# Optimization experiments

Measured on AMD Instinct MI355X. Metric: run time of the kernel, lower is better.

Reference implementation:

```python
import jax, jax.numpy as jnp
import numpy as np

FEAT_DIM = 2048
NUM_CLASSES = 1000
BATCH = 8192
REACH_SCALE = 10.0
COS_SCALE = 16.0


def setup_inputs() -> dict:
    key = jax.random.key(0)
    ks = jax.random.split(key, 7)
    x = jax.random.normal(ks[0], (BATCH, FEAT_DIM), dtype=jnp.float32)
    centroids = jax.random.normal(ks[1], (NUM_CLASSES, FEAT_DIM), dtype=jnp.float32)
    # nn.Linear-style params (W: [out, in], b: [out]), small init scale
    s_h = 1.0 / np.sqrt(FEAT_DIM)
    W_hall = jax.random.uniform(ks[2], (NUM_CLASSES, FEAT_DIM), jnp.float32, -s_h, s_h)
    b_hall = jax.random.uniform(ks[3], (NUM_CLASSES,), jnp.float32, -s_h, s_h)
    W_sel = jax.random.uniform(ks[4], (FEAT_DIM, FEAT_DIM), jnp.float32, -s_h, s_h)
    b_sel = jax.random.uniform(ks[5], (FEAT_DIM,), jnp.float32, -s_h, s_h)
    # CosNorm_Classifier weight: [num_classes, feat_dim]
    W_cos = jax.random.uniform(ks[6], (NUM_CLASSES, FEAT_DIM), jnp.float32, -s_h, s_h)
    return {"x": x, "centroids": centroids, "W_hall": W_hall, "b_hall": b_hall,
            "W_sel": W_sel, "b_sel": b_sel, "W_cos": W_cos}


def reference(x, centroids, W_hall, b_hall, W_sel, b_sel, W_cos):
    # --- min Euclidean distance to centroids via the matmul identity ---
    x_sq = jnp.sum(x * x, axis=1, keepdims=True)               # [B, 1]
    c_sq = jnp.sum(centroids * centroids, axis=1)[None, :]     # [1, C]
    d2 = x_sq + c_sq - 2.0 * (x @ centroids.T)                 # [B, C]
    min_dist = jnp.sqrt(jnp.maximum(jnp.min(d2, axis=1), 0.0)) # [B]
    reachability = (REACH_SCALE / min_dist)[:, None]           # [B, 1] (broadcasts over feat)

    # --- hallucinated memory attention over class centroids ---
    values_memory = jax.nn.softmax(x @ W_hall.T + b_hall, axis=1)  # [B, C]
    memory_feature = values_memory @ centroids                     # [B, D]

    # --- gated fusion ---
    concept_selector = jnp.tanh(x @ W_sel.T + b_sel)               # [B, D]
    infused_feature = concept_selector * memory_feature            # [B, D]
    fused = reachability * (x + infused_feature)                   # [B, D]

    # --- CosNorm classifier: scale * (|x|/(1+|x|)) * (x/|x|) @ (W/|W|)^T ---
    norm_x = jnp.linalg.norm(fused, axis=1, keepdims=True)         # [B, 1]
    ex = (norm_x / (1.0 + norm_x)) * (fused / norm_x)              # [B, D]
    ew = W_cos / jnp.linalg.norm(W_cos, axis=1, keepdims=True)     # [C, D]
    logits = COS_SCALE * (ex @ ew.T)                               # [B, C]

    direct_feature = x
    return logits, direct_feature, infused_feature
```

## Files before the change

kernel.cpp:

```cpp
#include <hip/hip_runtime.h>
#include <hip/hip_bf16.h>

typedef __bf16 bf16x8 __attribute__((ext_vector_type(8)));
typedef float  f32x4  __attribute__((ext_vector_type(4)));
typedef unsigned short u16;

__device__ __forceinline__ u16 f2bf(float f) {
    __hip_bfloat16 h = __float2bfloat16(f);
    return __builtin_bit_cast(unsigned short, h);
}
__device__ __forceinline__ float bf2f(u16 u) {
    return __bfloat162float(__builtin_bit_cast(__hip_bfloat16, u));
}

template <int MODE>
__device__ __forceinline__ float blockReduce(float v, float* sbuf) {
    #pragma unroll
    for (int off = 32; off > 0; off >>= 1) {
        float o = __shfl_down(v, off, 64);
        v = (MODE == 0) ? v + o : (MODE == 1) ? fmaxf(v, o) : fminf(v, o);
    }
    int lane = threadIdx.x & 63, w = threadIdx.x >> 6;
    __syncthreads();
    if (lane == 0) sbuf[w] = v;
    __syncthreads();
    float r = sbuf[0];
    #pragma unroll
    for (int i = 1; i < 4; ++i) {
        float o = sbuf[i];
        r = (MODE == 0) ? r + o : (MODE == 1) ? fmaxf(r, o) : fminf(r, o);
    }
    return r;
}

__global__ void convert_x(const float* __restrict__ src, u16* __restrict__ dst,
                          float* __restrict__ rowsq, float* __restrict__ copyOut,
                          float* __restrict__ scaleAcc) {
    __shared__ float sbuf[4];
    int r = blockIdx.x, t = threadIdx.x;
    size_t base = (size_t)r * 2048 + t * 8;
    float4 a0 = *(const float4*)(src + base);
    float4 a1 = *(const float4*)(src + base + 4);
    float ss = a0.x*a0.x + a0.y*a0.y + a0.z*a0.z + a0.w*a0.w
             + a1.x*a1.x + a1.y*a1.y + a1.z*a1.z + a1.w*a1.w;
    ushort4 u0, u1;
    u0.x = f2bf(a0.x); u0.y = f2bf(a0.y); u0.z = f2bf(a0.z); u0.w = f2bf(a0.w);
    u1.x = f2bf(a1.x); u1.y = f2bf(a1.y); u1.z = f2bf(a1.z); u1.w = f2bf(a1.w);
    *(ushort4*)(dst + base)     = u0;
    *(ushort4*)(dst + base + 4) = u1;
    *(float4*)(copyOut + base)     = a0;
    *(float4*)(copyOut + base + 4) = a1;
    ss = blockReduce<0>(ss, sbuf);
    if (t == 0) {
        rowsq[r] = ss;
        scaleAcc[r] = 0.f;
    }
}

__global__ void convert_weights(const float* __restrict__ cent, const float* __restrict__ whall,
                                const float* __restrict__ wsel, u16* __restrict__ Bp,
                                float* __restrict__ csq,
                                const float* __restrict__ wcos, u16* __restrict__ ew) {
    __shared__ float sbuf[4];
    int r = blockIdx.x, t = threadIdx.x;
    if (r >= 4096) {
        int rr = r - 4096;
        size_t base = (size_t)rr * 2048 + t * 8;
        ushort4 u0 = {0,0,0,0}, u1 = {0,0,0,0};
        if (rr < 1000) {
            float4 a0 = *(const float4*)(wcos + base);
            float4 a1 = *(const float4*)(wcos + base + 4);
            float ss = a0.x*a0.x + a0.y*a0.y + a0.z*a0.z + a0.w*a0.w
                     + a1.x*a1.x + a1.y*a1.y + a1.z*a1.z + a1.w*a1.w;
            ss = blockReduce<0>(ss, sbuf);
            float sc = 1.f / sqrtf(ss);
            u0.x = f2bf(a0.x*sc); u0.y = f2bf(a0.y*sc); u0.z = f2bf(a0.z*sc); u0.w = f2bf(a0.w*sc);
            u1.x = f2bf(a1.x*sc); u1.y = f2bf(a1.y*sc); u1.z = f2bf(a1.z*sc); u1.w = f2bf(a1.w*sc);
        }
        *(ushort4*)(ew + base)     = u0;
        *(ushort4*)(ew + base + 4) = u1;
        return;
    }
    const float* src; int sr; bool valid;
    if (r < 1024)       { src = cent;  sr = r;        valid = sr < 1000; }
    else if (r < 2048)  { src = whall; sr = r - 1024; valid = sr < 1000; }
    else                { src = wsel;  sr = r - 2048; valid = true; }
    size_t dbase = (size_t)r * 2048 + t * 8;
    float ss = 0.f;
    ushort4 u0 = {0,0,0,0}, u1 = {0,0,0,0};
    if (valid) {
        size_t sbase = (size_t)sr * 2048 + t * 8;
        float4 a0 = *(const float4*)(src + sbase);
        float4 a1 = *(const float4*)(src + sbase + 4);
        ss = a0.x*a0.x + a0.y*a0.y + a0.z*a0.z + a0.w*a0.w
           + a1.x*a1.x + a1.y*a1.y + a1.z*a1.z + a1.w*a1.w;
        u0.x = f2bf(a0.x); u0.y = f2bf(a0.y); u0.z = f2bf(a0.z); u0.w = f2bf(a0.w);
        u1.x = f2bf(a1.x); u1.y = f2bf(a1.y); u1.z = f2bf(a1.z); u1.w = f2bf(a1.w);
    }
    *(ushort4*)(Bp + dbase)     = u0;
    *(ushort4*)(Bp + dbase + 4) = u1;
    if (r < 1024) {
        ss = blockReduce<0>(ss, sbuf);
        if (t == 0) csq[r] = ss;
    }
}

__global__ void transpose_to_bf16(const float* __restrict__ src, u16* __restrict__ dst, int validRows) {
    __shared__ u16 tile[32][33];
    int d0 = blockIdx.x * 32;
    int c0 = blockIdx.y * 32;
    int tx = threadIdx.x, ty = threadIdx.y;
    #pragma unroll
    for (int k = 0; k < 4; ++k) {
        int c = c0 + ty + k * 8;
        float v = (c < validRows) ? src[(size_t)c * 2048 + d0 + tx] : 0.f;
        tile[ty + k * 8][tx] = f2bf(v);
    }
    __syncthreads();
    #pragma unroll
    for (int k = 0; k < 4; ++k) {
        int d = d0 + ty + k * 8;
        dst[(size_t)d * 1024 + c0 + tx] = tile[tx][ty + k * 8];
    }
}

template <int EPI>
__global__ __launch_bounds__(256, 4)
void gemm_bt(const u16* __restrict__ A, const u16* __restrict__ Bt,
             float* __restrict__ Cf, u16* __restrict__ Cb,
             int K, int ldc, int nValid,
             const float* __restrict__ bias,
             const u16* __restrict__ selp, int ldsel,
             const float* __restrict__ reach, const u16* __restrict__ xh2,
             u16* __restrict__ fusedh, float* __restrict__ scaleAcc) {
    __shared__ u16 As[128 * 64];
    __shared__ u16 Bs[128 * 64];
    const int tid  = threadIdx.x;
    const int lane = tid & 63;
    const int w    = tid >> 6;
    const int wr   = w >> 1, wc = w & 1;
    const int quad = lane >> 4, r16 = lane & 15;
    const int sw   = r16 & 7;
    const int lr   = lane >> 3;
    const int lc   = lane & 7;
    const int lk   = (lc ^ lr) * 8;
    const size_t rowBase = (size_t)blockIdx.y * 128;
    const size_t colBase = (size_t)blockIdx.x * 128;

    f32x4 acc[4][4] = {};

    for (int kt = 0; kt < K; kt += 64) {
        #pragma unroll
        for (int i = 0; i < 4; ++i) {
            int ci = w * 4 + i;
            const u16* ga = A  + (rowBase + ci * 8 + lr) * (size_t)K + kt + lk;
            const u16* gb = Bt + (colBase + ci * 8 + lr) * (size_t)K + kt + lk;
            __builtin_amdgcn_global_load_lds(
                (const __attribute__((address_space(1))) void*)ga,
                (__attribute__((address_space(3))) void*)(As + ci * 512), 16, 0, 0);
            __builtin_amdgcn_global_load_lds(
                (const __attribute__((address_space(1))) void*)gb,
                (__attribute__((address_space(3))) void*)(Bs + ci * 512), 16, 0, 0);
        }
        __syncthreads();
        #pragma unroll
        for (int kk2 = 0; kk2 < 2; ++kk2) {
            const int off = (((kk2 << 2) | quad) ^ sw) * 8;
            bf16x8 a[4], b[4];
            #pragma unroll
            for (int i = 0; i < 4; ++i)
                a[i] = *(const bf16x8*)(As + (wr * 64 + i * 16 + r16) * 64 + off);
            #pragma unroll
            for (int j = 0; j < 4; ++j)
                b[j] = *(const bf16x8*)(Bs + (wc * 64 + j * 16 + r16) * 64 + off);
            #pragma unroll
            for (int i = 0; i < 4; ++i)
                #pragma unroll
                for (int j = 0; j < 4; ++j)
                    acc[i][j] = __builtin_amdgcn_mfma_f32_16x16x32_bf16(a[i], b[j], acc[i][j], 0, 0, 0);
        }
        __syncthreads();
    }

    if (EPI == 2) {
        #pragma unroll
        for (int i = 0; i < 4; ++i) {
            #pragma unroll
            for (int v = 0; v < 4; ++v) {
                size_t grow = rowBase + wr * 64 + i * 16 + quad * 4 + v;
                float rch = reach[grow];
                float rs = 0.f;
                #pragma unroll
                for (int j = 0; j < 4; ++j) {
                    size_t gcol = colBase + wc * 64 + j * 16 + r16;
                    float val = acc[i][j][v];
                    float sv  = bf2f(selp[grow * (size_t)ldsel + gcol]);
                    float t   = tanhf(sv + bias[gcol]);
                    float inf = t * val;
                    Cf[grow * (size_t)ldc + gcol] = inf;
                    float xv = bf2f(xh2[grow * (size_t)ldc + gcol]);
                    float fs = rch * (xv + inf);
                    fusedh[grow * (size_t)ldc + gcol] = f2bf(fs);
                    rs += fs * fs;
                }
                #pragma unroll
                for (int off = 8; off > 0; off >>= 1)
                    rs += __shfl_down(rs, off, 16);
                if (r16 == 0) atomicAdd(&scaleAcc[grow], rs);
            }
        }
    } else {
        #pragma unroll
        for (int i = 0; i < 4; ++i) {
            #pragma unroll
            for (int j = 0; j < 4; ++j) {
                #pragma unroll
                for (int v = 0; v < 4; ++v) {
                    size_t grow = rowBase + wr * 64 + i * 16 + quad * 4 + v;
                    size_t gcol = colBase + wc * 64 + j * 16 + r16;
                    float val = acc[i][j][v];
                    if (EPI == 1) {
                        Cb[grow * (size_t)ldc + gcol] = f2bf(val);
                    } else if (EPI == 3) {
                        if ((int)gcol < nValid) {
                            float sc = 16.f / (1.f + sqrtf(bias[grow]));
                            Cf[grow * (size_t)ldc + gcol] = sc * val;
                        }
                    }
                }
            }
        }
    }
}

__global__ void min_softmax(const u16* __restrict__ Sp, const float* __restrict__ xsq,
                            const float* __restrict__ csq, const float* __restrict__ bh,
                            float* __restrict__ reach, u16* __restrict__ Vm) {
    __shared__ float sbuf[4];
    int r = blockIdx.x, t = threadIdx.x;
    size_t rb = (size_t)r * 4096;
    int c0 = t * 4;
    float m = 1e30f;
    if (t < 250) {
        ushort4 d4 = *(const ushort4*)(Sp + rb + c0);
        m = fminf(fminf(csq[c0+0] - 2.f * bf2f(d4.x), csq[c0+1] - 2.f * bf2f(d4.y)),
                  fminf(csq[c0+2] - 2.f * bf2f(d4.z), csq[c0+3] - 2.f * bf2f(d4.w)));
    }
    m = blockReduce<2>(m, sbuf);
    if (t == 0) {
        float d2 = xsq[r] + m;
        reach[r] = 10.f / sqrtf(fmaxf(d2, 0.f));
    }
    float l[4];
    float mx = -1e30f;
    if (t < 250) {
        ushort4 h4 = *(const ushort4*)(Sp + rb + 1024 + c0);
        l[0] = bf2f(h4.x) + bh[c0+0];
        l[1] = bf2f(h4.y) + bh[c0+1];
        l[2] = bf2f(h4.z) + bh[c0+2];
        l[3] = bf2f(h4.w) + bh[c0+3];
        mx = fmaxf(fmaxf(l[0], l[1]), fmaxf(l[2], l[3]));
    } else {
        l[0] = l[1] = l[2] = l[3] = -1e30f;
    }
    mx = blockReduce<1>(mx, sbuf);
    float s = 0.f;
    #pragma unroll
    for (int i = 0; i < 4; ++i) {
        l[i] = (t < 250) ? expf(l[i] - mx) : 0.f;
        s += l[i];
    }
    s = blockReduce<0>(s, sbuf);
    float inv = 1.f / s;
    ushort4 o;
    o.x = f2bf(l[0] * inv); o.y = f2bf(l[1] * inv);
    o.z = f2bf(l[2] * inv); o.w = f2bf(l[3] * inv);
    *(ushort4*)(Vm + (size_t)r * 1024 + c0) = o;
}

extern "C" void kernel_launch(void* const* d_in, const int* in_sizes, int n_in,
                              void* d_out, int out_size, void* d_ws, size_t ws_size,
                              hipStream_t stream) {
    const float* x      = (const float*)d_in[0];
    const float* cent   = (const float*)d_in[1];
    const float* W_hall = (const float*)d_in[2];
    const float* b_hall = (const float*)d_in[3];
    const float* W_sel  = (const float*)d_in[4];
    const float* b_sel  = (const float*)d_in[5];
    const float* W_cos  = (const float*)d_in[6];

    float* out_logits = (float*)d_out;
    float* out_x      = out_logits + (size_t)8192 * 1000;
    float* out_inf    = out_x      + (size_t)8192 * 2048;

    char* ws = (char*)d_ws;
    u16*   xh     = (u16*)  (ws);
    u16*   Bp     = (u16*)  (ws + 33554432);
    u16*   ew     = (u16*)  (ws + 50331648);
    u16*   centT  = (u16*)  (ws + 54525952);
    u16*   Sp     = (u16*)  (ws + 58720256);
    u16*   Vm     = (u16*)  (ws + 125829120);
    u16*   fusedh = (u16*)  (ws + 142606336);
    float* xsq    = (float*)(ws + 176160768);
    float* csq    = (float*)(ws + 176193536);
    float* reach  = (float*)(ws + 176197632);
    float* scale  = (float*)(ws + 176230400);

    (void)in_sizes; (void)n_in; (void)out_size; (void)ws_size;

    convert_x<<<8192, 256, 0, stream>>>(x, xh, xsq, out_x, scale);
    convert_weights<<<5120, 256, 0, stream>>>(cent, W_hall, W_sel, Bp, csq, W_cos, ew);
    transpose_to_bf16<<<dim3(64, 32), dim3(32, 8), 0, stream>>>(cent, centT, 1000);

    gemm_bt<1><<<dim3(32, 64), 256, 0, stream>>>(xh, Bp, nullptr, Sp, 2048, 4096, 0,
                                                 nullptr, nullptr, 0, nullptr, nullptr, nullptr, nullptr);
    min_softmax<<<8192, 256, 0, stream>>>(Sp, xsq, csq, b_hall, reach, Vm);

    gemm_bt<2><<<dim3(16, 64), 256, 0, stream>>>(Vm, centT, out_inf, nullptr, 1024, 2048, 0,
                                                 b_sel, Sp + 2048, 4096, reach, xh, fusedh, scale);

    gemm_bt<3><<<dim3(8, 64), 256, 0, stream>>>(fusedh, ew, out_logits, nullptr, 2048, 1000, 1000,
                                                scale, nullptr, 0, nullptr, nullptr, nullptr, nullptr);
}
```

Measured before the change: 516.8 us.

## Split-K the cosine classifier GEMM and use fast tanh/exp intrinsics

The final logits GEMM now splits K into two halves across blockIdx.z and accumulates partial results with float atomics. The logits buffer is zeroed beforehand inside the softmax kernel. This doubles the block count of a GEMM that previously ran only 512 blocks, to fill more CUs. It also replaces tanhf/expf with __expf-based fast versions and vectorizes the bias and csq loads, at some cost in accuracy, atomic traffic and nondeterministic summation order.

After: 567.9 us. 1.1x slower.

```diff
diff --git a/kernel.cpp b/kernel.cpp
--- a/kernel.cpp
+++ b/kernel.cpp
@@ -11,6 +11,10 @@
 }
 __device__ __forceinline__ float bf2f(u16 u) {
     return __bfloat162float(__builtin_bit_cast(__hip_bfloat16, u));
+}
+__device__ __forceinline__ float fast_tanh(float x) {
+    float e = __expf(2.f * x);
+    return 1.f - 2.f / (e + 1.f);
 }
 
 template <int MODE>
@@ -128,7 +132,7 @@
 __global__ __launch_bounds__(256, 4)
 void gemm_bt(const u16* __restrict__ A, const u16* __restrict__ Bt,
              float* __restrict__ Cf, u16* __restrict__ Cb,
-             int K, int ldc, int nValid,
+             int K, int lda, int ldc, int nValid,
              const float* __restrict__ bias,
              const u16* __restrict__ selp, int ldsel,
              const float* __restrict__ reach, const u16* __restrict__ xh2,
@@ -146,6 +150,7 @@
     const int lk   = (lc ^ lr) * 8;
     const size_t rowBase = (size_t)blockIdx.y * 128;
     const size_t colBase = (size_t)blockIdx.x * 128;
+    const int kOff = blockIdx.z * K;
 
     f32x4 acc[4][4] = {};
 
@@ -153,8 +158,8 @@
         #pragma unroll
         for (int i = 0; i < 4; ++i) {
             int ci = w * 4 + i;
-            const u16* ga = A  + (rowBase + ci * 8 + lr) * (size_t)K + kt + lk;
-            const u16* gb = Bt + (colBase + ci * 8 + lr) * (size_t)K + kt + lk;
+            const u16* ga = A  + (rowBase + ci * 8 + lr) * (size_t)lda + kOff + kt + lk;
+            const u16* gb = Bt + (colBase + ci * 8 + lr) * (size_t)lda + kOff + kt + lk;
             __builtin_amdgcn_global_load_lds(
                 (const __attribute__((address_space(1))) void*)ga,
                 (__attribute__((address_space(3))) void*)(As + ci * 512), 16, 0, 0);
@@ -195,7 +200,7 @@
                     size_t gcol = colBase + wc * 64 + j * 16 + r16;
                     float val = acc[i][j][v];
                     float sv  = bf2f(selp[grow * (size_t)ldsel + gcol]);
-                    float t   = tanhf(sv + bias[gcol]);
+                    float t   = fast_tanh(sv + bias[gcol]);
                     float inf = t * val;
                     Cf[grow * (size_t)ldc + gcol] = inf;
                     float xv = bf2f(xh2[grow * (size_t)ldc + gcol]);
@@ -224,7 +229,7 @@
                     } else if (EPI == 3) {
                         if ((int)gcol < nValid) {
                             float sc = 16.f / (1.f + sqrtf(bias[grow]));
-                            Cf[grow * (size_t)ldc + gcol] = sc * val;
+                            atomicAdd(&Cf[grow * (size_t)ldc + gcol], sc * val);
                         }
                     }
                 }
@@ -235,16 +240,22 @@
 
 __global__ void min_softmax(const u16* __restrict__ Sp, const float* __restrict__ xsq,
                             const float* __restrict__ csq, const float* __restrict__ bh,
-                            float* __restrict__ reach, u16* __restrict__ Vm) {
+                            float* __restrict__ reach, u16* __restrict__ Vm,
+                            float* __restrict__ outLog) {
     __shared__ float sbuf[4];
     int r = blockIdx.x, t = threadIdx.x;
     size_t rb = (size_t)r * 4096;
     int c0 = t * 4;
+    if (t < 250) {
+        float4 z = {0.f, 0.f, 0.f, 0.f};
+        *(float4*)(outLog + (size_t)r * 1000 + c0) = z;
+    }
     float m = 1e30f;
     if (t < 250) {
         ushort4 d4 = *(const ushort4*)(Sp + rb + c0);
-        m = fminf(fminf(csq[c0+0] - 2.f * bf2f(d4.x), csq[c0+1] - 2.f * bf2f(d4.y)),
-                  fminf(csq[c0+2] - 2.f * bf2f(d4.z), csq[c0+3] - 2.f * bf2f(d4.w)));
+        float4 cq = *(const float4*)(csq + c0);
+        m = fminf(fminf(cq.x - 2.f * bf2f(d4.x), cq.y - 2.f * bf2f(d4.y)),
+                  fminf(cq.z - 2.f * bf2f(d4.z), cq.w - 2.f * bf2f(d4.w)));
     }
     m = blockReduce<2>(m, sbuf);
     if (t == 0) {
@@ -255,10 +266,11 @@
     float mx = -1e30f;
     if (t < 250) {
         ushort4 h4 = *(const ushort4*)(Sp + rb + 1024 + c0);
-        l[0] = bf2f(h4.x) + bh[c0+0];
-        l[1] = bf2f(h4.y) + bh[c0+1];
-        l[2] = bf2f(h4.z) + bh[c0+2];
-        l[3] = bf2f(h4.w) + bh[c0+3];
+        float4 b4 = *(const float4*)(bh + c0);
+        l[0] = bf2f(h4.x) + b4.x;
+        l[1] = bf2f(h4.y) + b4.y;
+        l[2] = bf2f(h4.z) + b4.z;
+        l[3] = bf2f(h4.w) + b4.w;
         mx = fmaxf(fmaxf(l[0], l[1]), fmaxf(l[2], l[3]));
     } else {
         l[0] = l[1] = l[2] = l[3] = -1e30f;
@@ -267,7 +279,7 @@
     float s = 0.f;
     #pragma unroll
     for (int i = 0; i < 4; ++i) {
-        l[i] = (t < 250) ? expf(l[i] - mx) : 0.f;
+        l[i] = (t < 250) ? __expf(l[i] - mx) : 0.f;
         s += l[i];
     }
     s = blockReduce<0>(s, sbuf);
@@ -312,13 +324,13 @@
     convert_weights<<<5120, 256, 0, stream>>>(cent, W_hall, W_sel, Bp, csq, W_cos, ew);
     transpose_to_bf16<<<dim3(64, 32), dim3(32, 8), 0, stream>>>(cent, centT, 1000);
 
-    gemm_bt<1><<<dim3(32, 64), 256, 0, stream>>>(xh, Bp, nullptr, Sp, 2048, 4096, 0,
+    gemm_bt<1><<<dim3(32, 64), 256, 0, stream>>>(xh, Bp, nullptr, Sp, 2048, 2048, 4096, 0,
                                                  nullptr, nullptr, 0, nullptr, nullptr, nullptr, nullptr);
-    min_softmax<<<8192, 256, 0, stream>>>(Sp, xsq, csq, b_hall, reach, Vm);
-
-    gemm_bt<2><<<dim3(16, 64), 256, 0, stream>>>(Vm, centT, out_inf, nullptr, 1024, 2048, 0,
+    min_softmax<<<8192, 256, 0, stream>>>(Sp, xsq, csq, b_hall, reach, Vm, out_logits);
+
+    gemm_bt<2><<<dim3(16, 64), 256, 0, stream>>>(Vm, centT, out_inf, nullptr, 1024, 1024, 2048, 0,
                                                  b_sel, Sp + 2048, 4096, reach, xh, fusedh, scale);
 
-    gemm_bt<3><<<dim3(8, 64), 256, 0, stream>>>(fusedh, ew, out_logits, nullptr, 2048, 1000, 1000,
-                                                scale, nullptr, 0, nullptr, nullptr, nullptr, nullptr);
-}
+    gemm_bt<3><<<dim3(8, 64, 2), 256, 0, stream>>>(fusedh, ew, out_logits, nullptr, 1024, 2048, 1000, 1000,
+                                                   scale, nullptr, 0, nullptr, nullptr, nullptr, nullptr);
+}
```
